# Optimization experiments

Measured on AMD Instinct MI355X. Metric: run time of the kernel, lower is better.

## Reference

```python
import jax, jax.numpy as jnp
import numpy as np

N, E, C, L, NG = 50000, 600000, 128, 7, 512
EPS = 1e-7


def layer_norm(z, g, b):
    mu = z.mean(-1, keepdims=True)
    var = ((z - mu) ** 2).mean(-1, keepdims=True)
    return (z - mu) * jax.lax.rsqrt(var + 1e-5) * g + b


def setup_inputs() -> dict:
    key = jax.random.key(0)
    ks = jax.random.split(key, 16)
    inp = {
        'x': jax.random.randint(ks[0], (N, 9), 0, 64, dtype=jnp.int32),
        'edge_index': jax.random.randint(ks[1], (2, E), 0, N, dtype=jnp.int32),
        'edge_attr': jax.random.randint(ks[2], (E, 3), 0, 8, dtype=jnp.int32),
        'batch': jnp.sort(jax.random.randint(ks[3], (N,), 0, NG, dtype=jnp.int32)),
        'atom_emb': jax.random.normal(ks[4], (9, 64, C), jnp.float32) * 0.1,
        'bond_emb': jax.random.normal(ks[5], (3, 8, C), jnp.float32) * 0.1,
        'vn_emb': jnp.zeros((1, C), jnp.float32),
        'conv_W1': jax.random.normal(ks[6], (L, C, 2 * C), jnp.float32) / np.sqrt(C),
        'conv_b1': jnp.zeros((L, 2 * C), jnp.float32),
        'conv_g1': jnp.ones((L, 2 * C), jnp.float32),
        'conv_bb1': jnp.zeros((L, 2 * C), jnp.float32),
        'conv_W2': jax.random.normal(ks[7], (L, 2 * C, C), jnp.float32) / np.sqrt(2 * C),
        'conv_b2': jnp.zeros((L, C), jnp.float32),
        'norm_g': jnp.ones((L, C), jnp.float32),
        'norm_b': jnp.zeros((L, C), jnp.float32),
        'vn_W1': jax.random.normal(ks[8], (L - 1, C, C), jnp.float32) / np.sqrt(C),
        'vn_b1': jnp.zeros((L - 1, C), jnp.float32),
        'vn_g': jnp.ones((L - 1, C), jnp.float32),
        'vn_bb': jnp.zeros((L - 1, C), jnp.float32),
        'vn_W2': jax.random.normal(ks[9], (L - 1, C, C), jnp.float32) / np.sqrt(C),
        'vn_b2': jnp.zeros((L - 1, C), jnp.float32),
    }
    return inp


def reference(x, edge_index, edge_attr, batch, atom_emb, bond_emb, vn_emb,
              conv_W1, conv_b1, conv_g1, conv_bb1, conv_W2, conv_b2,
              norm_g, norm_b, vn_W1, vn_b1, vn_g, vn_bb, vn_W2, vn_b2):
    src, dst = edge_index[0], edge_index[1]

    # AtomEncoder: sum of per-feature embeddings -> [N, C]
    h = atom_emb[jnp.arange(9), x].sum(axis=1)
    # BondEncoder (conv_encode_edge=False) -> [E, C]
    edge_emb = bond_emb[jnp.arange(3), edge_attr].sum(axis=1)

    # virtual node embedding (one per graph)
    vn = jnp.broadcast_to(vn_emb[0], (NG, C))
    h = h + vn[batch]

    def gen_conv(l, hx):
        # GENConv: msg = relu(x_j + e) + eps; softmax aggregation (t=1); MLP(x+m)
        msg = jax.nn.relu(hx[src] + edge_emb) + EPS                      # [E, C]
        mx = jax.ops.segment_max(msg, dst, num_segments=N)               # [N, C]
        e = jnp.exp(msg - mx[dst])
        den = jax.ops.segment_sum(e, dst, num_segments=N)
        m = jax.ops.segment_sum(msg * (e / (den[dst] + 1e-16)), dst, num_segments=N)
        z = hx + m
        z = jax.nn.relu(layer_norm(z @ conv_W1[l] + conv_b1[l], conv_g1[l], conv_bb1[l]))
        return z @ conv_W2[l] + conv_b2[l]

    # res+ block: Conv -> [Norm -> ReLU -> (VN update) -> Conv + res]*
    h = gen_conv(0, h)
    for l in range(1, L):
        h2 = jax.nn.relu(layer_norm(h, norm_g[l - 1], norm_b[l - 1]))
        vtmp = jax.ops.segment_sum(h2, batch, num_segments=NG) + vn
        v = jax.nn.relu(layer_norm(vtmp @ vn_W1[l - 1] + vn_b1[l - 1], vn_g[l - 1], vn_bb[l - 1]))
        vn = v @ vn_W2[l - 1] + vn_b2[l - 1]
        h2 = h2 + vn[batch]
        h = gen_conv(l, h2) + h
    h = layer_norm(h, norm_g[L - 1], norm_b[L - 1])

    # global_add_pool -> [NG, C]
    return jax.ops.segment_sum(h, batch, num_segments=NG)
```

## Files before the change

### kernel.cpp

```cpp
#include <hip/hip_runtime.h>
#include <hip/hip_bf16.h>
#include <stdint.h>

#define N_NODES 50000
#define N_EDGES 600000
#define CH 128
#define NLAYERS 7
#define NGRAPHS 512

typedef __hip_bfloat16 bf16;
using bf16x8 = __attribute__((ext_vector_type(8))) __bf16;
using f32x4  = __attribute__((ext_vector_type(4))) float;

static __device__ __forceinline__ float b2f(bf16 v){ return __bfloat162float(v); }

__global__ void k_detect(const uint32_t* __restrict__ g, int* __restrict__ flag){
  if (threadIdx.x == 0 && blockIdx.x == 0) flag[0] = (g[0] == 0x3F803F80u) ? 1 : 0;
}

struct Segs { const void* src[12]; float* dst[12]; int n[12]; };

__global__ void k_cvt_all(const int* __restrict__ flag, Segs S){
  int f = flag[0];
  int seg = blockIdx.y;
  int n = S.n[seg];
  const void* src = S.src[seg];
  float* dst = S.dst[seg];
  for (int i = blockIdx.x*blockDim.x + threadIdx.x; i < n; i += gridDim.x*blockDim.x)
    dst[i] = f ? b2f(((const bf16*)src)[i]) : ((const float*)src)[i];
}

__global__ void k_transpose_all(const int* __restrict__ flag,
    const void* W1, const void* W2, const void* vW1, const void* vW2,
    bf16* W1p, bf16* W2T, bf16* vW1p, bf16* vW2T){
  int f = flag[0];
  const int T0 = NLAYERS*128*256, T1 = NLAYERS*256*128;
  const int T2 = (NLAYERS-1)*128*128;
  int total = T0+T1+2*T2;
  for (int i = blockIdx.x*blockDim.x + threadIdx.x; i < total; i += gridDim.x*blockDim.x){
    float v;
    if (i < T0){
      int idx = i; int l = idx/(128*256); int rem = idx - l*128*256; int k = rem >> 8; int n = rem & 255;
      v = f ? b2f(((const bf16*)W1)[idx]) : ((const float*)W1)[idx];
      W1p[(size_t)l*256*128 + n*128 + (k ^ ((n&7)<<3))] = __float2bfloat16(v);
    } else if (i < T0+T1){
      int idx = i-T0; int l = idx/(256*128); int rem = idx - l*256*128; int k = rem >> 7; int n = rem & 127;
      v = f ? b2f(((const bf16*)W2)[idx]) : ((const float*)W2)[idx];
      W2T[(size_t)l*128*256 + n*256 + k] = __float2bfloat16(v);
    } else if (i < T0+T1+T2){
      int idx = i-T0-T1; int l = idx/(128*128); int rem = idx - l*128*128; int k = rem >> 7; int n = rem & 127;
      v = f ? b2f(((const bf16*)vW1)[idx]) : ((const float*)vW1)[idx];
      vW1p[(size_t)l*128*128 + n*128 + (k ^ ((n&7)<<3))] = __float2bfloat16(v);
    } else {
      int idx = i-T0-T1-T2; int l = idx/(128*128); int rem = idx - l*128*128; int k = rem >> 7; int n = rem & 127;
      v = f ? b2f(((const bf16*)vW2)[idx]) : ((const float*)vW2)[idx];
      vW2T[(size_t)l*128*128 + n*128 + k] = __float2bfloat16(v);
    }
  }
}

__global__ void k_bondC(const int* __restrict__ flag, const void* __restrict__ bond,
                        float* __restrict__ bondC){
  int f = flag[0];
  int i = blockIdx.x*blockDim.x + threadIdx.x;
  if (i >= 512*128) return;
  int idx = i >> 7, c = i & 127;
  int a0 = idx & 7, a1 = (idx>>3) & 7, a2 = (idx>>6) & 7;
  auto g = [&](int e)->float{ return f ? b2f(((const bf16*)bond)[e]) : ((const float*)bond)[e]; };
  bondC[i] = g((0*8+a0)*128 + c) + g((1*8+a1)*128 + c) + g((2*8+a2)*128 + c);
}

__global__ void k_zero_i32(int* p, int n){
  for (int i = blockIdx.x*blockDim.x + threadIdx.x; i < n; i += gridDim.x*blockDim.x) p[i] = 0;
}

__global__ void k_hist(const int* __restrict__ keys, int* __restrict__ counts, int n){
  for (int i = blockIdx.x*blockDim.x + threadIdx.x; i < n; i += gridDim.x*blockDim.x)
    atomicAdd(&counts[keys[i]], 1);
}

__global__ __launch_bounds__(256) void k_scanA(const int* __restrict__ in, int* __restrict__ out,
                                               int* __restrict__ bsums, int n){
  __shared__ int lds[256];
  int t = threadIdx.x;
  int base = blockIdx.x * 1024;
  int v[4]; int s = 0;
  #pragma unroll
  for (int i=0;i<4;i++){ int idx = base + t*4 + i; int x = (idx<n)? in[idx] : 0; v[i]=x; s+=x; }
  lds[t] = s; __syncthreads();
  for (int off=1; off<256; off<<=1){
    int x = (t>=off)? lds[t-off] : 0;
    __syncthreads();
    lds[t] += x;
    __syncthreads();
  }
  int p = lds[t] - s;
  #pragma unroll
  for (int i=0;i<4;i++){ int idx = base + t*4 + i; if (idx<n) out[idx] = p; p += v[i]; }
  if (t==255) bsums[blockIdx.x] = lds[255];
}

__global__ __launch_bounds__(256) void k_scanB(int* bsums, int nblk){
  __shared__ int lds[256];
  int t = threadIdx.x;
  int v = (t<nblk)? bsums[t] : 0;
  lds[t] = v; __syncthreads();
  for (int off=1; off<256; off<<=1){
    int x = (t>=off)? lds[t-off] : 0;
    __syncthreads();
    lds[t] += x;
    __syncthreads();
  }
  if (t<nblk) bsums[t] = lds[t] - v;
}

__global__ void k_scanC(int* out, const int* bsums, int n){
  for (int i = blockIdx.x*blockDim.x + threadIdx.x; i < n; i += gridDim.x*blockDim.x)
    out[i] += bsums[i >> 10];
}

__global__ void k_scatter(const int* __restrict__ ei, const int* __restrict__ ea,
                          const int* __restrict__ row_ptr, int* __restrict__ fill,
                          uint32_t* __restrict__ csr){
  for (int e = blockIdx.x*blockDim.x + threadIdx.x; e < N_EDGES; e += gridDim.x*blockDim.x){
    int src = ei[e];
    int dst = ei[N_EDGES + e];
    int pos = row_ptr[dst] + atomicAdd(&fill[dst], 1);
    uint32_t a0 = (uint32_t)ea[e*3+0], a1 = (uint32_t)ea[e*3+1], a2 = (uint32_t)ea[e*3+2];
    csr[pos] = (uint32_t)src | ((a0 | (a1<<3) | (a2<<6)) << 16);
  }
}

__global__ void k_gptr(const int* __restrict__ batch, int* __restrict__ gptr){
  int i = blockIdx.x*blockDim.x + threadIdx.x;
  if (i >= N_NODES) return;
  int b = batch[i];
  if (i == 0){ for (int g=0; g<=b; ++g) gptr[g] = 0; }
  else { int bp = batch[i-1]; for (int g=bp+1; g<=b; ++g) gptr[g] = i; }
  if (i == N_NODES-1){ for (int g=b+1; g<=NGRAPHS; ++g) gptr[g] = N_NODES; }
}

__global__ __launch_bounds__(128) void k_atom_encode(const int* __restrict__ x,
    const float* __restrict__ atom_emb, const float* __restrict__ vn_emb,
    uint32_t* __restrict__ hxb){
  int n = blockIdx.x; int c = threadIdx.x;
  float s = vn_emb[c];
  #pragma unroll
  for (int f=0; f<9; ++f){
    int xv = x[n*9+f];
    s += atom_emb[(f*64 + xv)*CH + c];
  }
  float o = __shfl_xor(s, 1);
  if ((c & 1) == 0){
    __hip_bfloat162 p; p.x = __float2bfloat16(s); p.y = __float2bfloat16(o);
    hxb[n*64 + (c>>1)] = *reinterpret_cast<uint32_t*>(&p);
  }
}

__global__ void k_vn_init(const float* __restrict__ vn_emb, float* __restrict__ vn){
  for (int i = blockIdx.x*blockDim.x + threadIdx.x; i < NGRAPHS*CH; i += gridDim.x*blockDim.x)
    vn[i] = vn_emb[i & (CH-1)];
}

__global__ __launch_bounds__(64) void k_aggregate(const uint32_t* __restrict__ hxb,
     const uint32_t* __restrict__ csr, const int* __restrict__ row_ptr,
     const float* __restrict__ bondC, uint32_t* __restrict__ z){
  int n = blockIdx.x; int t = threadIdx.x;
  int s0 = row_ptr[n], s1 = row_ptr[n+1];
  float sa=0.f, sb=0.f, wa=0.f, wb=0.f;
  int i = s0;
  for (; i+4 <= s1; i += 4){
    uint32_t u0=csr[i], u1=csr[i+1], u2=csr[i+2], u3=csr[i+3];
    uint32_t h0 = hxb[(size_t)(u0 & 0xFFFFu)*64 + t];
    uint32_t h1 = hxb[(size_t)(u1 & 0xFFFFu)*64 + t];
    uint32_t h2 = hxb[(size_t)(u2 & 0xFFFFu)*64 + t];
    uint32_t h3 = hxb[(size_t)(u3 & 0xFFFFu)*64 + t];
    float2 c0 = *reinterpret_cast<const float2*>(bondC + (size_t)(u0 >> 16)*128 + 2*t);
    float2 c1 = *reinterpret_cast<const float2*>(bondC + (size_t)(u1 >> 16)*128 + 2*t);
    float2 c2 = *reinterpret_cast<const float2*>(bondC + (size_t)(u2 >> 16)*128 + 2*t);
    float2 c3 = *reinterpret_cast<const float2*>(bondC + (size_t)(u3 >> 16)*128 + 2*t);
    #define EDGE(hp, bc) { \
      float va = __uint_as_float(hp << 16) + bc.x; \
      float vb = __uint_as_float(hp & 0xFFFF0000u) + bc.y; \
      va = fmaxf(va, 0.f) + 1e-7f; vb = fmaxf(vb, 0.f) + 1e-7f; \
      float pa = __expf(va - 10.f), pb = __expf(vb - 10.f); \
      sa += pa; wa += pa*va; sb += pb; wb += pb*vb; }
    EDGE(h0, c0) EDGE(h1, c1) EDGE(h2, c2) EDGE(h3, c3)
  }
  for (; i < s1; ++i){
    uint32_t u = csr[i];
    uint32_t hp = hxb[(size_t)(u & 0xFFFFu)*64 + t];
    float2 bc = *reinterpret_cast<const float2*>(bondC + (size_t)(u >> 16)*128 + 2*t);
    EDGE(hp, bc)
    #undef EDGE
  }
  uint32_t own = hxb[(size_t)n*64 + t];
  float za = __uint_as_float(own << 16)         + wa/(sa + 1e-16f);
  float zb = __uint_as_float(own & 0xFFFF0000u) + wb/(sb + 1e-16f);
  __hip_bfloat162 p; p.x = __float2bfloat16(za); p.y = __float2bfloat16(zb);
  z[(size_t)n*64 + (t ^ ((n&7)<<2))] = *reinterpret_cast<uint32_t*>(&p);
}

template<int K, int N1, int N2>
__global__ __launch_bounds__(512, 2) void k_mlp6(const bf16* __restrict__ A,
    const bf16* __restrict__ W1s,
    const float* __restrict__ b1, const float* __restrict__ g1, const float* __restrict__ bb1,
    const bf16* __restrict__ W2T,
    const float* __restrict__ b2,
    const float* __restrict__ residual, float* __restrict__ out, int M, int NT)
{
  constexpr int KK1 = K/32;
  constexpr int WC  = N1/4;
  constexpr int JC  = WC/16;
  constexpr int KK2 = N1/32;
  constexpr int W1E = N1*K;
  constexpr int AE  = 64*K;
  constexpr int ZE  = 64*N1;
  __shared__ __align__(16) bf16 W1L[W1E];
  __shared__ __align__(16) bf16 AL[AE];
  __shared__ __align__(16) bf16 zt[ZE];
  __shared__ float lnp[64][4][2];
  __shared__ float lnv[64][2];

  const int tid = threadIdx.x;
  const int wid = tid >> 6, lane = tid & 63;
  const int wr = wid >> 2, wc = wid & 3;
  const int rlo = lane & 15, hi = lane >> 4, khi = hi*8;

  {
    constexpr int NC_ = (W1E*2)/1024/8;
    #pragma unroll
    for (int c=0;c<NC_;++c){
      int cc = c*8 + wid;
      __builtin_amdgcn_global_load_lds((const uint32_t*)((const char*)W1s + cc*1024 + lane*16),
                                       (uint32_t*)((char*)W1L + cc*1024), 16, 0, 0);
    }
  }
  float b1v[JC], gv[JC], bbv[JC];
  #pragma unroll
  for (int jc=0;jc<JC;++jc){
    int col = wc*WC + jc*16 + rlo;
    b1v[jc] = b1[col]; gv[jc] = g1[col]; bbv[jc] = bb1[col];
  }
  float bv2[2] = { b2[wc*32 + rlo], b2[wc*32 + 16 + rlo] };

  for (int t = blockIdx.x; ; ){
    {
      const char* src = (const char*)A + (size_t)t*AE*2;
      constexpr int NCA = (AE*2)/1024/8;
      #pragma unroll
      for (int c=0;c<NCA;++c){
        int cc = c*8 + wid;
        __builtin_amdgcn_global_load_lds((const uint32_t*)(src + cc*1024 + lane*16),
                                         (uint32_t*)((char*)AL + cc*1024), 16, 0, 0);
      }
    }
    __syncthreads();

    f32x4 acc1[2][JC];
    #pragma unroll
    for (int rt=0;rt<2;++rt)
      #pragma unroll
      for (int jc=0;jc<JC;++jc) acc1[rt][jc] = {0.f,0.f,0.f,0.f};
    #pragma unroll
    for (int kk=0;kk<KK1;++kk){
      bf16x8 af[2], bw[JC];
      #pragma unroll
      for (int rt=0;rt<2;++rt){
        int lr = wr*32 + rt*16 + rlo;
        af[rt] = *reinterpret_cast<const bf16x8*>(&AL[lr*K + ((kk*32 + khi) ^ ((lr&7)<<3))]);
      }
      #pragma unroll
      for (int jc=0;jc<JC;++jc){
        int n = wc*WC + jc*16 + rlo;
        bw[jc] = *reinterpret_cast<const bf16x8*>(&W1L[n*K + ((kk*32 + khi) ^ ((n&7)<<3))]);
      }
      #pragma unroll
      for (int rt=0;rt<2;++rt)
        #pragma unroll
        for (int jc=0;jc<JC;++jc)
          acc1[rt][jc] = __builtin_amdgcn_mfma_f32_16x16x32_bf16(af[rt], bw[jc], acc1[rt][jc], 0,0,0);
    }

    bf16x8 B2f[2][KK2];
    #pragma unroll
    for (int ct=0;ct<2;++ct){
      const bf16* wp = W2T + (size_t)(wc*32 + ct*16 + rlo)*N1 + khi;
      #pragma unroll
      for (int kk=0;kk<KK2;++kk)
        B2f[ct][kk] = *reinterpret_cast<const bf16x8*>(wp + kk*32);
    }
    float resv[2][2][4];
    if (residual){
      #pragma unroll
      for (int rt=0;rt<2;++rt)
        #pragma unroll
        for (int r=0;r<4;++r){
          int grow = t*64 + wr*32 + rt*16 + hi*4 + r; if (grow >= M) grow = M-1;
          #pragma unroll
          for (int ct=0;ct<2;++ct)
            resv[rt][ct][r] = residual[(size_t)grow*N2 + wc*32 + ct*16 + rlo];
        }
    }
    __builtin_amdgcn_sched_barrier(0);

    float p[2][4], q[2][4];
    #pragma unroll
    for (int rt=0;rt<2;++rt)
      #pragma unroll
      for (int r=0;r<4;++r){ p[rt][r]=0.f; q[rt][r]=0.f; }
    #pragma unroll
    for (int jc=0;jc<JC;++jc)
      #pragma unroll
      for (int rt=0;rt<2;++rt)
        #pragma unroll
        for (int r=0;r<4;++r){
          float v = acc1[rt][jc][r] + b1v[jc]; acc1[rt][jc][r] = v;
          p[rt][r] += v; q[rt][r] += v*v;
        }
    #pragma unroll
    for (int rt=0;rt<2;++rt)
      #pragma unroll
      for (int r=0;r<4;++r){
        float pv = p[rt][r], qv = q[rt][r];
        #pragma unroll
        for (int off=1; off<16; off<<=1){ pv += __shfl_xor(pv, off); qv += __shfl_xor(qv, off); }
        if (rlo == 0){
          int row = wr*32 + rt*16 + hi*4 + r;
          lnp[row][wc][0] = pv; lnp[row][wc][1] = qv;
        }
      }
    __syncthreads();
    if (tid < 64){
      float P=0.f, Q=0.f;
      #pragma unroll
      for (int w=0;w<4;++w){ P += lnp[tid][w][0]; Q += lnp[tid][w][1]; }
      float mu = P*(1.f/N1);
      lnv[tid][0] = mu;
      lnv[tid][1] = rsqrtf(Q*(1.f/N1) - mu*mu + 1e-5f);
    }
    __syncthreads();

    #pragma unroll
    for (int rt=0;rt<2;++rt)
      #pragma unroll
      for (int r=0;r<4;++r){
        int row = wr*32 + rt*16 + hi*4 + r;
        float mu = lnv[row][0], rs = lnv[row][1];
        #pragma unroll
        for (int jc=0;jc<JC;++jc){
          int col = wc*WC + jc*16 + rlo;
          float y = (acc1[rt][jc][r]-mu)*rs*gv[jc] + bbv[jc];
          zt[row*N1 + (col ^ ((row&7)<<3))] = __float2bfloat16(fmaxf(y, 0.f));
        }
      }
    __syncthreads();

    f32x4 acc2[2][2];
    #pragma unroll
    for (int rt=0;rt<2;++rt)
      #pragma unroll
      for (int ct=0;ct<2;++ct) acc2[rt][ct] = {0.f,0.f,0.f,0.f};
    #pragma unroll
    for (int kk=0;kk<KK2;++kk){
      bf16x8 a2[2];
      #pragma unroll
      for (int rt=0;rt<2;++rt){
        int row = wr*32 + rt*16 + rlo;
        a2[rt] = *reinterpret_cast<const bf16x8*>(&zt[row*N1 + ((kk*32 + khi) ^ ((row&7)<<3))]);
      }
      #pragma unroll
      for (int rt=0;rt<2;++rt)
        #pragma unroll
        for (int ct=0;ct<2;++ct)
          acc2[rt][ct] = __builtin_amdgcn_mfma_f32_16x16x32_bf16(a2[rt], B2f[ct][kk], acc2[rt][ct], 0,0,0);
    }
    #pragma unroll
    for (int ct=0;ct<2;++ct)
      #pragma unroll
      for (int rt=0;rt<2;++rt)
        #pragma unroll
        for (int r=0;r<4;++r){
          int grow = t*64 + wr*32 + rt*16 + hi*4 + r;
          if (grow < M){
            float v = acc2[rt][ct][r] + bv2[ct];
            if (residual) v += resv[rt][ct][r];
            out[(size_t)grow*N2 + wc*32 + ct*16 + rlo] = v;
          }
        }

    t += (int)gridDim.x;
    if (t >= NT) break;
    __syncthreads();
  }
}

__global__ __launch_bounds__(256) void k_ln_row(const float* __restrict__ in,
    const float* __restrict__ g, const float* __restrict__ b,
    float* __restrict__ outF, int rows, int relu)
{
  int wid = threadIdx.x >> 6, lane = threadIdx.x & 63;
  int row = blockIdx.x*4 + wid;
  if (row >= rows) return;
  const float* p = in + (size_t)row*CH;
  float x0 = p[lane], x1 = p[64+lane];
  float s = x0 + x1;
  #pragma unroll
  for (int off=32; off; off>>=1) s += __shfl_xor(s, off);
  float mu = s * (1.0f/CH);
  float d0 = x0-mu, d1 = x1-mu;
  float vs = d0*d0 + d1*d1;
  #pragma unroll
  for (int off=32; off; off>>=1) vs += __shfl_xor(vs, off);
  float rstd = rsqrtf(vs*(1.0f/CH) + 1e-5f);
  float y0 = d0*rstd*g[lane] + b[lane];
  float y1 = d1*rstd*g[64+lane] + b[64+lane];
  if (relu){ y0 = fmaxf(y0,0.f); y1 = fmaxf(y1,0.f); }
  outF[(size_t)row*CH + lane] = y0;
  outF[(size_t)row*CH + 64 + lane] = y1;
}

__global__ void k_vncopy(const float* __restrict__ vn, float* __restrict__ vnacc){
  int i = blockIdx.x*blockDim.x + threadIdx.x;
  if (i < NGRAPHS*CH) vnacc[i] = vn[i];
}

__global__ void k_prep_vtb(const float* __restrict__ vnacc, bf16* __restrict__ vtb){
  int i = blockIdx.x*blockDim.x + threadIdx.x;
  if (i < NGRAPHS*CH){
    int g = i >> 7, k = i & 127;
    vtb[g*128 + (k ^ ((g&7)<<3))] = __float2bfloat16(vnacc[i]);
  }
}

#define SEGC 128
__global__ __launch_bounds__(128) void k_segsum2(const float* __restrict__ hx,
    const int* __restrict__ batch, float* __restrict__ vnacc){
  int c = threadIdx.x;
  int n0 = blockIdx.x*SEGC;
  int n1 = n0 + SEGC; if (n1 > N_NODES) n1 = N_NODES;
  if (n0 >= N_NODES) return;
  int cur = batch[n0];
  float s = 0.f;
  for (int n = n0; n < n1; ++n){
    int b = batch[n];
    if (b != cur){ atomicAdd(&vnacc[cur*CH + c], s); s = 0.f; cur = b; }
    s += hx[(size_t)n*CH + c];
  }
  atomicAdd(&vnacc[cur*CH + c], s);
}

__global__ void k_add_vn(const float* __restrict__ hx, const float* __restrict__ vn,
                         const int* __restrict__ batch, uint32_t* __restrict__ hxb){
  for (int i = blockIdx.x*blockDim.x + threadIdx.x; i < N_NODES*64; i += gridDim.x*blockDim.x){
    int n = i >> 6; int t = i & 63;
    float2 hv = *reinterpret_cast<const float2*>(hx + (size_t)n*CH + 2*t);
    float2 vv = *reinterpret_cast<const float2*>(vn + (size_t)batch[n]*CH + 2*t);
    __hip_bfloat162 p; p.x = __float2bfloat16(hv.x+vv.x); p.y = __float2bfloat16(hv.y+vv.y);
    hxb[i] = *reinterpret_cast<uint32_t*>(&p);
  }
}

__global__ __launch_bounds__(128) void k_pool(const float* __restrict__ hx,
    const int* __restrict__ gptr, const int* __restrict__ flag, void* __restrict__ out){
  int g = blockIdx.x; int c = threadIdx.x;
  float s = 0.f;
  for (int n = gptr[g]; n < gptr[g+1]; ++n) s += hx[(size_t)n*CH + c];
  if (flag[0]) ((bf16*)out)[g*CH+c] = __float2bfloat16(s);
  else         ((float*)out)[g*CH+c] = s;
}

extern "C" void kernel_launch(void* const* d_in, const int* in_sizes, int n_in,
                              void* d_out, int out_size, void* d_ws, size_t ws_size,
                              hipStream_t stream)
{
  const int*  x     = (const int*) d_in[0];
  const int*  ei    = (const int*) d_in[1];
  const int*  ea    = (const int*) d_in[2];
  const int*  batch = (const int*) d_in[3];
  const void* atom_emb = d_in[4];
  const void* bond_emb = d_in[5];
  const void* vn_emb   = d_in[6];
  const void* conv_W1  = d_in[7];
  const void* conv_b1  = d_in[8];
  const void* conv_g1  = d_in[9];
  const void* conv_bb1 = d_in[10];
  const void* conv_W2  = d_in[11];
  const void* conv_b2  = d_in[12];
  const void* norm_g   = d_in[13];
  const void* norm_b   = d_in[14];
  const void* vn_W1    = d_in[15];
  const void* vn_b1    = d_in[16];
  const void* vn_g     = d_in[17];
  const void* vn_bb    = d_in[18];
  const void* vn_W2    = d_in[19];
  const void* vn_b2    = d_in[20];

  char* wsb = (char*)d_ws;
  size_t off = 0;
  auto alloc = [&](size_t bytes)->char*{ char* p = wsb + off; off += (bytes + 255) & ~(size_t)255; return p; };
  const int ZROWS = 50048;
  float*    h     = (float*)   alloc(sizeof(float)*N_NODES*CH);
  float*    hx    = (float*)   alloc(sizeof(float)*N_NODES*CH);
  uint32_t* hxb   = (uint32_t*)alloc(sizeof(uint32_t)*N_NODES*64);
  uint32_t* z     = (uint32_t*)alloc(sizeof(uint32_t)*ZROWS*64);
  float*    vn    = (float*)   alloc(sizeof(float)*NGRAPHS*CH);
  float*    vnacc = (float*)   alloc(sizeof(float)*NGRAPHS*CH);
  bf16*     vtb   = (bf16*)    alloc(sizeof(bf16)*NGRAPHS*CH);
  bf16*     W1Tp  = (bf16*)    alloc(sizeof(bf16)*NLAYERS*256*128);
  bf16*     W2T   = (bf16*)    alloc(sizeof(bf16)*NLAYERS*128*256);
  bf16*     vW1Tp = (bf16*)    alloc(sizeof(bf16)*(NLAYERS-1)*128*128);
  bf16*     vW2T  = (bf16*)    alloc(sizeof(bf16)*(NLAYERS-1)*128*128);
  int* row_ptr = (int*)alloc(sizeof(int)*(N_NODES+1));
  int* counts  = (int*)alloc(sizeof(int)*(N_NODES+1));
  uint32_t* csr = (uint32_t*)alloc(sizeof(uint32_t)*N_EDGES);
  int* gptr    = (int*)alloc(sizeof(int)*(NGRAPHS+1));
  int* bsums   = (int*)alloc(sizeof(int)*256);
  int* flag    = (int*)alloc(sizeof(int)*64);
  float* atomF = (float*)alloc(sizeof(float)*9*64*CH);
  float* bondC = (float*)alloc(sizeof(float)*512*CH);
  float* vnEF  = (float*)alloc(sizeof(float)*CH);
  float* b1F   = (float*)alloc(sizeof(float)*NLAYERS*2*CH);
  float* g1F   = (float*)alloc(sizeof(float)*NLAYERS*2*CH);
  float* bb1F  = (float*)alloc(sizeof(float)*NLAYERS*2*CH);
  float* b2F   = (float*)alloc(sizeof(float)*NLAYERS*CH);
  float* ngF   = (float*)alloc(sizeof(float)*NLAYERS*CH);
  float* nbF   = (float*)alloc(sizeof(float)*NLAYERS*CH);
  float* vb1F  = (float*)alloc(sizeof(float)*(NLAYERS-1)*CH);
  float* vgF   = (float*)alloc(sizeof(float)*(NLAYERS-1)*CH);
  float* vbbF  = (float*)alloc(sizeof(float)*(NLAYERS-1)*CH);
  float* vb2F  = (float*)alloc(sizeof(float)*(NLAYERS-1)*CH);

  k_detect<<<1, 64, 0, stream>>>((const uint32_t*)norm_g, flag);
  Segs S;
  int si = 0;
  auto seg = [&](const void* s_, float* d_, int n_){ S.src[si]=s_; S.dst[si]=d_; S.n[si]=n_; ++si; };
  seg(atom_emb, atomF, 9*64*CH);
  seg(vn_emb,   vnEF,  CH);
  seg(conv_b1,  b1F,  NLAYERS*2*CH);
  seg(conv_g1,  g1F,  NLAYERS*2*CH);
  seg(conv_bb1, bb1F, NLAYERS*2*CH);
  seg(conv_b2,  b2F,  NLAYERS*CH);
  seg(norm_g,   ngF,  NLAYERS*CH);
  seg(norm_b,   nbF,  NLAYERS*CH);
  seg(vn_b1,    vb1F, (NLAYERS-1)*CH);
  seg(vn_g,     vgF,  (NLAYERS-1)*CH);
  seg(vn_bb,    vbbF, (NLAYERS-1)*CH);
  seg(vn_b2,    vb2F, (NLAYERS-1)*CH);
  k_cvt_all<<<dim3(72, 12), 256, 0, stream>>>(flag, S);
  k_transpose_all<<<640, 256, 0, stream>>>(flag, conv_W1, conv_W2, vn_W1, vn_W2,
                                           W1Tp, W2T, vW1Tp, vW2T);
  k_bondC<<<256, 256, 0, stream>>>(flag, bond_emb, bondC);

  k_zero_i32<<<64, 256, 0, stream>>>(counts, N_NODES+1);
  k_hist<<<512, 256, 0, stream>>>(ei + N_EDGES, counts, N_EDGES);
  int nblkE = (N_NODES+1 + 1023)/1024;
  k_scanA<<<nblkE, 256, 0, stream>>>(counts, row_ptr, bsums, N_NODES+1);
  k_scanB<<<1, 256, 0, stream>>>(bsums, nblkE);
  k_scanC<<<64, 256, 0, stream>>>(row_ptr, bsums, N_NODES+1);
  k_zero_i32<<<64, 256, 0, stream>>>(counts, N_NODES+1);
  k_scatter<<<512, 256, 0, stream>>>(ei, ea, row_ptr, counts, csr);
  k_gptr<<<(N_NODES+255)/256, 256, 0, stream>>>(batch, gptr);

  k_atom_encode<<<N_NODES, 128, 0, stream>>>(x, atomF, vnEF, hxb);
  k_vn_init<<<64, 256, 0, stream>>>(vnEF, vn);

  int lnBlocksN = (N_NODES + 3)/4;
  const int NT_CONV = (N_NODES + 63)/64;
  const int NT_VN   = NGRAPHS/64;

  for (int l = 0; l < NLAYERS; ++l){
    if (l > 0){
      k_ln_row<<<lnBlocksN, 256, 0, stream>>>(h, ngF + (l-1)*CH, nbF + (l-1)*CH, hx, N_NODES, 1);
      k_vncopy<<<(NGRAPHS*CH+255)/256, 256, 0, stream>>>(vn, vnacc);
      k_segsum2<<<(N_NODES+SEGC-1)/SEGC, 128, 0, stream>>>(hx, batch, vnacc);
      k_prep_vtb<<<(NGRAPHS*CH+255)/256, 256, 0, stream>>>(vnacc, vtb);
      k_mlp6<128,128,128><<<NT_VN, 512, 0, stream>>>(vtb,
          vW1Tp + (size_t)(l-1)*128*128, vb1F + (l-1)*CH, vgF + (l-1)*CH, vbbF + (l-1)*CH,
          vW2T + (size_t)(l-1)*128*128, vb2F + (l-1)*CH, nullptr, vn, NGRAPHS, NT_VN);
      k_add_vn<<<1024, 256, 0, stream>>>(hx, vn, batch, hxb);
    }
    k_aggregate<<<N_NODES, 64, 0, stream>>>(hxb, csr, row_ptr, bondC, z);
    k_mlp6<128,256,128><<<256, 512, 0, stream>>>((const bf16*)z,
        W1Tp + (size_t)l*256*128, b1F + l*2*CH, g1F + l*2*CH, bb1F + l*2*CH,
        W2T + (size_t)l*128*256, b2F + l*CH, (l==0)? nullptr : h, h, N_NODES, NT_CONV);
  }
  k_ln_row<<<lnBlocksN, 256, 0, stream>>>(h, ngF + (NLAYERS-1)*CH, nbF + (NLAYERS-1)*CH,
                                          hx, N_NODES, 0);
  k_pool<<<NGRAPHS, 128, 0, stream>>>(hx, gptr, flag, d_out);
}
```

Baseline: 989.6 us.

## Fuse row LayerNorm into conv MLP epilogue and double-buffer A tiles

The conv MLP kernel now also computes the following LayerNorm (with optional ReLU) on its output rows and writes hx directly, which removes the separate k_ln_row pass and its full re-read of h. The A tile is double-buffered so the next tile's global-to-LDS load is issued while the current tile computes. W2 fragments are hoisted out of the tile loop into registers, and the VN MLP converts fp32 input itself instead of going through k_prep_vtb. In exchange the kernel uses more LDS and registers, which could lower occupancy, and it adds LDS-only barriers in the epilogue.

```diff
diff --git a/kernel.cpp b/kernel.cpp
--- a/kernel.cpp
+++ b/kernel.cpp
@@ -11,8 +11,15 @@
 typedef __hip_bfloat16 bf16;
 using bf16x8 = __attribute__((ext_vector_type(8))) __bf16;
 using f32x4  = __attribute__((ext_vector_type(4))) float;
+using u32x4  = __attribute__((ext_vector_type(4))) uint32_t;
 
 static __device__ __forceinline__ float b2f(bf16 v){ return __bfloat162float(v); }
+
+static __device__ __forceinline__ void bar_lds(){
+  asm volatile("s_waitcnt lgkmcnt(0)" ::: "memory");
+  __builtin_amdgcn_sched_barrier(0);
+  __builtin_amdgcn_s_barrier();
+}
 
 __global__ void k_detect(const uint32_t* __restrict__ g, int* __restrict__ flag){
   if (threadIdx.x == 0 && blockIdx.x == 0) flag[0] = (g[0] == 0x3F803F80u) ? 1 : 0;
@@ -201,24 +208,24 @@
   z[(size_t)n*64 + (t ^ ((n&7)<<2))] = *reinterpret_cast<uint32_t*>(&p);
 }
 
-template<int K, int N1, int N2>
-__global__ __launch_bounds__(512, 2) void k_mlp6(const bf16* __restrict__ A,
+template<int K, int N1, int N2, bool VNIN>
+__global__ __launch_bounds__(512, 2) void k_mlp7(const bf16* __restrict__ A,
+    const float* __restrict__ Af32,
     const bf16* __restrict__ W1s,
     const float* __restrict__ b1, const float* __restrict__ g1, const float* __restrict__ bb1,
     const bf16* __restrict__ W2T,
     const float* __restrict__ b2,
-    const float* __restrict__ residual, float* __restrict__ out, int M, int NT)
+    const float* __restrict__ lng, const float* __restrict__ lnb,
+    const float* __restrict__ residual, float* __restrict__ out,
+    float* __restrict__ hxout, int relu2, int M, int NT)
 {
   constexpr int KK1 = K/32;
   constexpr int WC  = N1/4;
   constexpr int JC  = WC/16;
   constexpr int KK2 = N1/32;
-  constexpr int W1E = N1*K;
-  constexpr int AE  = 64*K;
-  constexpr int ZE  = 64*N1;
-  __shared__ __align__(16) bf16 W1L[W1E];
-  __shared__ __align__(16) bf16 AL[AE];
-  __shared__ __align__(16) bf16 zt[ZE];
+  __shared__ __align__(16) bf16 W1L[N1*K];
+  __shared__ __align__(16) bf16 AL[2][64*K];
+  __shared__ __align__(16) bf16 zt[64*N1];
   __shared__ float lnp[64][4][2];
   __shared__ float lnv[64][2];
 
@@ -228,7 +235,7 @@
   const int rlo = lane & 15, hi = lane >> 4, khi = hi*8;
 
   {
-    constexpr int NC_ = (W1E*2)/1024/8;
+    constexpr int NC_ = (N1*K*2)/1024/8;
     #pragma unroll
     for (int c=0;c<NC_;++c){
       int cc = c*8 + wid;
@@ -236,6 +243,7 @@
                                        (uint32_t*)((char*)W1L + cc*1024), 16, 0, 0);
     }
   }
+
   float b1v[JC], gv[JC], bbv[JC];
   #pragma unroll
   for (int jc=0;jc<JC;++jc){
@@ -243,19 +251,54 @@
     b1v[jc] = b1[col]; gv[jc] = g1[col]; bbv[jc] = bb1[col];
   }
   float bv2[2] = { b2[wc*32 + rlo], b2[wc*32 + 16 + rlo] };
-
-  for (int t = blockIdx.x; ; ){
-    {
-      const char* src = (const char*)A + (size_t)t*AE*2;
-      constexpr int NCA = (AE*2)/1024/8;
+  float lngv[2] = {0.f,0.f}, lnbv[2] = {0.f,0.f};
+  if (hxout){
+    lngv[0] = lng[wc*32 + rlo];      lnbv[0] = lnb[wc*32 + rlo];
+    lngv[1] = lng[wc*32 + 16 + rlo]; lnbv[1] = lnb[wc*32 + 16 + rlo];
+  }
+  u32x4 b2raw[2][KK2];
+  #pragma unroll
+  for (int ct=0;ct<2;++ct){
+    const bf16* wp = W2T + (size_t)(wc*32 + ct*16 + rlo)*N1 + khi;
+    #pragma unroll
+    for (int kk=0;kk<KK2;++kk){
+      b2raw[ct][kk] = *reinterpret_cast<const u32x4*>(wp + kk*32);
+      asm volatile("" : "+v"(b2raw[ct][kk]));
+    }
+  }
+
+  auto stageA = [&](int nb, int tile){
+    if constexpr (!VNIN){
+      const char* src = (const char*)A + (size_t)tile*(64*K*2);
+      constexpr int NCA = (64*K*2)/1024/8;
       #pragma unroll
       for (int c=0;c<NCA;++c){
         int cc = c*8 + wid;
         __builtin_amdgcn_global_load_lds((const uint32_t*)(src + cc*1024 + lane*16),
-                                         (uint32_t*)((char*)AL + cc*1024), 16, 0, 0);
-      }
-    }
-    __syncthreads();
+                                         (uint32_t*)((char*)&AL[nb][0] + cc*1024), 16, 0, 0);
+      }
+    } else {
+      int base = tile*64;
+      #pragma unroll
+      for (int e=0;e<(64*K/4)/512;++e){
+        int idx = tid + e*512;
+        int row = idx >> 5;
+        int k4  = (idx & 31)*4;
+        float4 v = *reinterpret_cast<const float4*>(Af32 + (size_t)(base+row)*K + k4);
+        int s = (row&7)<<3;
+        bf16* d = &AL[nb][row*K + (k4 ^ s)];
+        d[0]=__float2bfloat16(v.x); d[1]=__float2bfloat16(v.y);
+        d[2]=__float2bfloat16(v.z); d[3]=__float2bfloat16(v.w);
+      }
+    }
+  };
+
+  int t = blockIdx.x, buf = 0;
+  stageA(0, t);
+  __syncthreads();
+
+  while (true){
+    int tn = t + (int)gridDim.x;
 
     f32x4 acc1[2][JC];
     #pragma unroll
@@ -268,7 +311,7 @@
       #pragma unroll
       for (int rt=0;rt<2;++rt){
         int lr = wr*32 + rt*16 + rlo;
-        af[rt] = *reinterpret_cast<const bf16x8*>(&AL[lr*K + ((kk*32 + khi) ^ ((lr&7)<<3))]);
+        af[rt] = *reinterpret_cast<const bf16x8*>(&AL[buf][lr*K + ((kk*32 + khi) ^ ((lr&7)<<3))]);
       }
       #pragma unroll
       for (int jc=0;jc<JC;++jc){
@@ -282,14 +325,7 @@
           acc1[rt][jc] = __builtin_amdgcn_mfma_f32_16x16x32_bf16(af[rt], bw[jc], acc1[rt][jc], 0,0,0);
     }
 
-    bf16x8 B2f[2][KK2];
-    #pragma unroll
-    for (int ct=0;ct<2;++ct){
-      const bf16* wp = W2T + (size_t)(wc*32 + ct*16 + rlo)*N1 + khi;
-      #pragma unroll
-      for (int kk=0;kk<KK2;++kk)
-        B2f[ct][kk] = *reinterpret_cast<const bf16x8*>(wp + kk*32);
-    }
+    if (tn < NT) stageA(buf^1, tn);
     float resv[2][2][4];
     if (residual){
       #pragma unroll
@@ -330,7 +366,7 @@
           lnp[row][wc][0] = pv; lnp[row][wc][1] = qv;
         }
       }
-    __syncthreads();
+    bar_lds();
     if (tid < 64){
       float P=0.f, Q=0.f;
       #pragma unroll
@@ -339,7 +375,7 @@
       lnv[tid][0] = mu;
       lnv[tid][1] = rsqrtf(Q*(1.f/N1) - mu*mu + 1e-5f);
     }
-    __syncthreads();
+    bar_lds();
 
     #pragma unroll
     for (int rt=0;rt<2;++rt)
@@ -354,7 +390,7 @@
           zt[row*N1 + (col ^ ((row&7)<<3))] = __float2bfloat16(fmaxf(y, 0.f));
         }
       }
-    __syncthreads();
+    bar_lds();
 
     f32x4 acc2[2][2];
     #pragma unroll
@@ -372,65 +408,78 @@
       #pragma unroll
       for (int rt=0;rt<2;++rt)
         #pragma unroll
-        for (int ct=0;ct<2;++ct)
-          acc2[rt][ct] = __builtin_amdgcn_mfma_f32_16x16x32_bf16(a2[rt], B2f[ct][kk], acc2[rt][ct], 0,0,0);
-    }
-    #pragma unroll
-    for (int ct=0;ct<2;++ct)
+        for (int ct=0;ct<2;++ct){
+          bf16x8 bb;
+          __builtin_memcpy(&bb, &b2raw[ct][kk], 16);
+          acc2[rt][ct] = __builtin_amdgcn_mfma_f32_16x16x32_bf16(a2[rt], bb, acc2[rt][ct], 0,0,0);
+        }
+    }
+
+    float vmat[2][2][4];
+    #pragma unroll
+    for (int rt=0;rt<2;++rt)
+      #pragma unroll
+      for (int ct=0;ct<2;++ct)
+        #pragma unroll
+        for (int r=0;r<4;++r){
+          float v = acc2[rt][ct][r] + bv2[ct];
+          if (residual) v += resv[rt][ct][r];
+          vmat[rt][ct][r] = v;
+          int grow = t*64 + wr*32 + rt*16 + hi*4 + r;
+          if (grow < M) out[(size_t)grow*N2 + wc*32 + ct*16 + rlo] = v;
+        }
+
+    if (hxout){
       #pragma unroll
       for (int rt=0;rt<2;++rt)
         #pragma unroll
         for (int r=0;r<4;++r){
-          int grow = t*64 + wr*32 + rt*16 + hi*4 + r;
+          float pv = vmat[rt][0][r] + vmat[rt][1][r];
+          float qv = vmat[rt][0][r]*vmat[rt][0][r] + vmat[rt][1][r]*vmat[rt][1][r];
+          #pragma unroll
+          for (int off=1; off<16; off<<=1){ pv += __shfl_xor(pv, off); qv += __shfl_xor(qv, off); }
+          if (rlo == 0){
+            int row = wr*32 + rt*16 + hi*4 + r;
+            lnp[row][wc][0] = pv; lnp[row][wc][1] = qv;
+          }
+        }
+      bar_lds();
+      if (tid < 64){
+        float P=0.f, Q=0.f;
+        #pragma unroll
+        for (int w=0;w<4;++w){ P += lnp[tid][w][0]; Q += lnp[tid][w][1]; }
+        float mu = P*(1.f/N2);
+        lnv[tid][0] = mu;
+        lnv[tid][1] = rsqrtf(Q*(1.f/N2) - mu*mu + 1e-5f);
+      }
+      bar_lds();
+      #pragma unroll
+      for (int rt=0;rt<2;++rt)
+        #pragma unroll
+        for (int r=0;r<4;++r){
+          int row = wr*32 + rt*16 + hi*4 + r;
+          float mu = lnv[row][0], rs = lnv[row][1];
+          int grow = t*64 + row;
           if (grow < M){
-            float v = acc2[rt][ct][r] + bv2[ct];
-            if (residual) v += resv[rt][ct][r];
-            out[(size_t)grow*N2 + wc*32 + ct*16 + rlo] = v;
+            #pragma unroll
+            for (int ct=0;ct<2;++ct){
+              float y = (vmat[rt][ct][r]-mu)*rs*lngv[ct] + lnbv[ct];
+              if (relu2) y = fmaxf(y, 0.f);
+              hxout[(size_t)grow*N2 + wc*32 + ct*16 + rlo] = y;
+            }
           }
         }
-
-    t += (int)gridDim.x;
-    if (t >= NT) break;
+    }
+
+    if (tn >= NT) break;
+    t = tn; buf ^= 1;
     __syncthreads();
   }
-}
-
-__global__ __launch_bounds__(256) void k_ln_row(const float* __restrict__ in,
-    const float* __restrict__ g, const float* __restrict__ b,
-    float* __restrict__ outF, int rows, int relu)
-{
-  int wid = threadIdx.x >> 6, lane = threadIdx.x & 63;
-  int row = blockIdx.x*4 + wid;
-  if (row >= rows) return;
-  const float* p = in + (size_t)row*CH;
-  float x0 = p[lane], x1 = p[64+lane];
-  float s = x0 + x1;
-  #pragma unroll
-  for (int off=32; off; off>>=1) s += __shfl_xor(s, off);
-  float mu = s * (1.0f/CH);
-  float d0 = x0-mu, d1 = x1-mu;
-  float vs = d0*d0 + d1*d1;
-  #pragma unroll
-  for (int off=32; off; off>>=1) vs += __shfl_xor(vs, off);
-  float rstd = rsqrtf(vs*(1.0f/CH) + 1e-5f);
-  float y0 = d0*rstd*g[lane] + b[lane];
-  float y1 = d1*rstd*g[64+lane] + b[64+lane];
-  if (relu){ y0 = fmaxf(y0,0.f); y1 = fmaxf(y1,0.f); }
-  outF[(size_t)row*CH + lane] = y0;
-  outF[(size_t)row*CH + 64 + lane] = y1;
 }
 
 __global__ void k_vncopy(const float* __restrict__ vn, float* __restrict__ vnacc){
   int i = blockIdx.x*blockDim.x + threadIdx.x;
   if (i < NGRAPHS*CH) vnacc[i] = vn[i];
-}
-
-__global__ void k_prep_vtb(const float* __restrict__ vnacc, bf16* __restrict__ vtb){
-  int i = blockIdx.x*blockDim.x + threadIdx.x;
-  if (i < NGRAPHS*CH){
-    int g = i >> 7, k = i & 127;
-    vtb[g*128 + (k ^ ((g&7)<<3))] = __float2bfloat16(vnacc[i]);
-  }
 }
 
 #define SEGC 128
@@ -506,7 +555,6 @@
   uint32_t* z     = (uint32_t*)alloc(sizeof(uint32_t)*ZROWS*64);
   float*    vn    = (float*)   alloc(sizeof(float)*NGRAPHS*CH);
   float*    vnacc = (float*)   alloc(sizeof(float)*NGRAPHS*CH);
-  bf16*     vtb   = (bf16*)    alloc(sizeof(bf16)*NGRAPHS*CH);
   bf16*     W1Tp  = (bf16*)    alloc(sizeof(bf16)*NLAYERS*256*128);
   bf16*     W2T   = (bf16*)    alloc(sizeof(bf16)*NLAYERS*128*256);
   bf16*     vW1Tp = (bf16*)    alloc(sizeof(bf16)*(NLAYERS-1)*128*128);
@@ -565,27 +613,25 @@
   k_atom_encode<<<N_NODES, 128, 0, stream>>>(x, atomF, vnEF, hxb);
   k_vn_init<<<64, 256, 0, stream>>>(vnEF, vn);
 
-  int lnBlocksN = (N_NODES + 3)/4;
   const int NT_CONV = (N_NODES + 63)/64;
   const int NT_VN   = NGRAPHS/64;
 
   for (int l = 0; l < NLAYERS; ++l){
     if (l > 0){
-      k_ln_row<<<lnBlocksN, 256, 0, stream>>>(h, ngF + (l-1)*CH, nbF + (l-1)*CH, hx, N_NODES, 1);
       k_vncopy<<<(NGRAPHS*CH+255)/256, 256, 0, stream>>>(vn, vnacc);
       k_segsum2<<<(N_NODES+SEGC-1)/SEGC, 128, 0, stream>>>(hx, batch, vnacc);
-      k_prep_vtb<<<(NGRAPHS*CH+255)/256, 256, 0, stream>>>(vnacc, vtb);
-      k_mlp6<128,128,128><<<NT_VN, 512, 0, stream>>>(vtb,
+      k_mlp7<128,128,128,true><<<NT_VN, 512, 0, stream>>>(nullptr, vnacc,
           vW1Tp + (size_t)(l-1)*128*128, vb1F + (l-1)*CH, vgF + (l-1)*CH, vbbF + (l-1)*CH,
-          vW2T + (size_t)(l-1)*128*128, vb2F + (l-1)*CH, nullptr, vn, NGRAPHS, NT_VN);
+          vW2T + (size_t)(l-1)*128*128, vb2F + (l-1)*CH,
+          nullptr, nullptr, nullptr, vn, nullptr, 0, NGRAPHS, NT_VN);
       k_add_vn<<<1024, 256, 0, stream>>>(hx, vn, batch, hxb);
     }
     k_aggregate<<<N_NODES, 64, 0, stream>>>(hxb, csr, row_ptr, bondC, z);
-    k_mlp6<128,256,128><<<256, 512, 0, stream>>>((const bf16*)z,
+    k_mlp7<128,256,128,false><<<256, 512, 0, stream>>>((const bf16*)z, nullptr,
         W1Tp + (size_t)l*256*128, b1F + l*2*CH, g1F + l*2*CH, bb1F + l*2*CH,
-        W2T + (size_t)l*128*256, b2F + l*CH, (l==0)? nullptr : h, h, N_NODES, NT_CONV);
-  }
-  k_ln_row<<<lnBlocksN, 256, 0, stream>>>(h, ngF + (NLAYERS-1)*CH, nbF + (NLAYERS-1)*CH,
-                                          hx, N_NODES, 0);
+        W2T + (size_t)l*128*256, b2F + l*CH,
+        ngF + l*CH, nbF + l*CH,
+        (l==0)? nullptr : h, h, hx, (l < NLAYERS-1) ? 1 : 0, N_NODES, NT_CONV);
+  }
   k_pool<<<NGRAPHS, 128, 0, stream>>>(hx, gptr, flag, d_out);
 }
```

After: 965.8 us. 2.4% less time.
